# Kernel tuning notes

Measured on AMD Instinct MI355X. Metric: run time of the kernel, lower is better.

Reference implementation:

```python
import jax, jax.numpy as jnp
import numpy as np

B, Q, K, DQ, DK, DV, H = 4, 256, 1024, 512, 512, 512, 128
MASK_VALUE = -1e6  # matches torch sequence_mask fill of -1000000.0


def setup_inputs() -> dict:
    key = jax.random.key(0)
    ks = jax.random.split(key, 7)
    q = jax.random.normal(ks[0], (B, Q, DQ), dtype=jnp.float32)
    k = jax.random.normal(ks[1], (B, K, DK), dtype=jnp.float32)
    v = jax.random.normal(ks[2], (B, K, DV), dtype=jnp.float32)
    valid_lens = jax.random.randint(ks[3], (B,), 1, K + 1).astype(jnp.int64)
    # Linear weights stored torch-style as [out, in]
    w_q = jax.random.normal(ks[4], (H, DQ), dtype=jnp.float32) * 0.05
    w_k = jax.random.normal(ks[5], (H, DK), dtype=jnp.float32) * 0.05
    w_v = jax.random.normal(ks[6], (H,), dtype=jnp.float32) * 0.05
    return {"q": q, "k": k, "v": v, "valid_lens": valid_lens,
            "w_q": w_q, "w_k": w_k, "w_v": w_v}


def reference(q, k, v, valid_lens, w_q, w_k, w_v):
    qh = jnp.einsum("bqd,hd->bqh", q, w_q)              # [B,Q,H]
    kh = jnp.einsum("bkd,hd->bkh", k, w_k)              # [B,K,H]
    feats = jnp.tanh(qh[:, :, None, :] + kh[:, None, :, :])  # [B,Q,K,H]
    scores = jnp.einsum("bqkh,h->bqk", feats, w_v)      # [B,Q,K]
    mask = jnp.arange(K)[None, None, :] < valid_lens[:, None, None]
    scores = jnp.where(mask, scores, MASK_VALUE)
    attn = jax.nn.softmax(scores, axis=-1)              # dropout is identity (p=0)
    return jnp.einsum("bqk,bkv->bqv", attn, v)          # [B,Q,DV]
```

## Files before the change

### kernel.cpp

```cpp
#include <hip/hip_runtime.h>

#define B_ 4
#define Q_ 256
#define K_ 1024
#define D_ 512
#define H_ 128
#define DV_ 512
#define SCALE 2.885390081777927f
#define LOG2E 1.4426950408889634f
#define N2LOG2E (-2.0f * 1.4426950408889634f)

__device__ __forceinline__ float sigl(float x) {
    return __builtin_amdgcn_rcpf(__builtin_amdgcn_exp2f(x) + 1.0f);
}

__global__ __launch_bounds__(256) void transpose_w(
    const float* __restrict__ wq, const float* __restrict__ wk,
    float* __restrict__ wt_q, float* __restrict__ wt_k)
{
    __shared__ float Ts[64][133];
    const int t = threadIdx.x, bid = blockIdx.x;
    const int m = bid >> 3, d0 = (bid & 7) * 64;
    const float* W  = m ? wk : wq;
    float*       WT = m ? wt_k : wt_q;
#pragma unroll
    for (int i = 0; i < 8; ++i) {
        int idx = i * 256 + t;
        int h = idx >> 4, dq = idx & 15;
        float4 v = *(const float4*)&W[(size_t)h * D_ + d0 + dq*4];
        Ts[dq*4+0][h] = v.x; Ts[dq*4+1][h] = v.y;
        Ts[dq*4+2][h] = v.z; Ts[dq*4+3][h] = v.w;
    }
    __syncthreads();
#pragma unroll
    for (int i = 0; i < 8; ++i) {
        int idx = i * 256 + t;
        int d = idx >> 5, h4 = idx & 31;
        *(float4*)&WT[(size_t)(d0 + d) * H_ + h4*4] = *(const float4*)&Ts[d][h4*4];
    }
}

__global__ __launch_bounds__(256) void proj2_kernel(
    const float* __restrict__ qin, const float* __restrict__ kin,
    const float* __restrict__ wt_q, const float* __restrict__ wt_k,
    const int* __restrict__ valid_lens,
    float* __restrict__ qh_s, float4* __restrict__ kh4)
{
    __shared__ float Xs[16][512];

    const int t = threadIdx.x, bid = blockIdx.x;
    const bool isQ = bid < 64;
    const float* X; const float* WT; int R0; int b = 0;
    if (isQ) { X = qin; WT = wt_q; R0 = bid * 16; }
    else {
        int kb = bid - 64;
        b  = kb >> 6;
        R0 = (kb & 63) * 16;
        if (R0 >= valid_lens[b]) return;
        X = kin + (size_t)b * K_ * D_;
        WT = wt_k;
    }

#pragma unroll
    for (int i = 0; i < 8; ++i) {
        int idx = i * 256 + t;
        int row = idx >> 7, d4 = idx & 127;
        *(float4*)&Xs[row][d4*4] = *(const float4*)&X[(size_t)(R0 + row) * D_ + d4*4];
    }
    __syncthreads();

    const int h4 = t & 31, rg = t >> 5;
    const int r0 = rg * 2;
    float4 c0 = make_float4(0,0,0,0), c1 = c0;

    const float* WTh = WT + h4*4;
    float4 w0 = *(const float4*)&WTh[0*H_];
    float4 w1 = *(const float4*)&WTh[1*H_];
    float4 w2 = *(const float4*)&WTh[2*H_];
    float4 w3 = *(const float4*)&WTh[3*H_];

#pragma unroll 2
    for (int d0 = 0; d0 < D_; d0 += 4) {
        float4 u0 = w0, u1 = w1, u2 = w2, u3 = w3;
        int dn = (d0 + 4 < D_) ? d0 + 4 : d0;
        w0 = *(const float4*)&WTh[(size_t)(dn+0) * H_];
        w1 = *(const float4*)&WTh[(size_t)(dn+1) * H_];
        w2 = *(const float4*)&WTh[(size_t)(dn+2) * H_];
        w3 = *(const float4*)&WTh[(size_t)(dn+3) * H_];
        float4 x0 = *(const float4*)&Xs[r0][d0];
        float4 x1 = *(const float4*)&Xs[r0+1][d0];
        c0.x += x0.x*u0.x + x0.y*u1.x + x0.z*u2.x + x0.w*u3.x;
        c0.y += x0.x*u0.y + x0.y*u1.y + x0.z*u2.y + x0.w*u3.y;
        c0.z += x0.x*u0.z + x0.y*u1.z + x0.z*u2.z + x0.w*u3.z;
        c0.w += x0.x*u0.w + x0.y*u1.w + x0.z*u2.w + x0.w*u3.w;
        c1.x += x1.x*u0.x + x1.y*u1.x + x1.z*u2.x + x1.w*u3.x;
        c1.y += x1.x*u0.y + x1.y*u1.y + x1.z*u2.y + x1.w*u3.y;
        c1.z += x1.x*u0.z + x1.y*u1.z + x1.z*u2.z + x1.w*u3.z;
        c1.w += x1.x*u0.w + x1.y*u1.w + x1.z*u2.w + x1.w*u3.w;
    }
    c0.x *= SCALE; c0.y *= SCALE; c0.z *= SCALE; c0.w *= SCALE;
    c1.x *= SCALE; c1.y *= SCALE; c1.z *= SCALE; c1.w *= SCALE;

    if (isQ) {
        *(float4*)&qh_s[(size_t)(R0 + r0)     * H_ + h4*4] = c0;
        *(float4*)&qh_s[(size_t)(R0 + r0 + 1) * H_ + h4*4] = c1;
    } else {
        kh4[(size_t)(b*32 + h4) * K_ + R0 + r0]     = c0;
        kh4[(size_t)(b*32 + h4) * K_ + R0 + r0 + 1] = c1;
    }
}

__global__ __launch_bounds__(256) void attn_part(
    const float* __restrict__ qh_s, const float4* __restrict__ kh4,
    const float* __restrict__ wvg,  const int* __restrict__ valid_lens,
    const float* __restrict__ vin,
    float* __restrict__ s_part, float4* __restrict__ o_part)
{
    __shared__ float  qv[512];
    __shared__ float  wvs[128];
    __shared__ float  ptmp[4][128];
    __shared__ float  p[4][128];
    __shared__ float  sred[2][4];
    __shared__ float4 otmp[4][128];

    const int t   = threadIdx.x;
    const int bid = blockIdx.x;
    const int qt  = bid & 63, b = (bid >> 6) & 3, kc = bid >> 8;
    const int q0  = qt * 4;
    const int vl  = valid_lens[b];
    const int kbase = kc * 128;
    if (kbase >= vl) return;
    const int klen = min(128, vl - kbase);

    qv[t]       = qh_s[(size_t)(b*Q_ + q0) * H_ + t];
    qv[t + 256] = qh_s[(size_t)(b*Q_ + q0) * H_ + t + 256];
    if (t < 128) wvs[t] = wvg[t];
    __syncthreads();

    const int k   = t & 127;
    const int hh  = t >> 7;
    const bool active = k < klen;

    float acc[4] = {0.f, 0.f, 0.f, 0.f};
    if (active) {
        const float4* khp = kh4 + (size_t)b * 32 * K_ + (kbase + k)
                          + (size_t)(hh * 16) * K_;
        const int hq0 = hh * 16;
        float4 kxn = khp[0];
#pragma unroll 4
        for (int i = 0; i < 16; ++i) {
            float4 kx = kxn;
            int ni = (i < 15) ? i + 1 : 15;
            kxn = khp[(size_t)ni * K_];
            const int hq = hq0 + i;
            float w4[4], q4[4][4];
            *(float4*)&w4[0] = *(const float4*)&wvs[hq*4];
#pragma unroll
            for (int qi = 0; qi < 4; ++qi)
                *(float4*)&q4[qi][0] = *(const float4*)&qv[qi*128 + hq*4];
            float kxa[4];
            *(float4*)&kxa[0] = kx;
#pragma unroll
            for (int j = 0; j < 4; ++j)
#pragma unroll
                for (int qi = 0; qi < 4; ++qi)
                    acc[qi] += w4[j] * sigl(q4[qi][j] + kxa[j]);
        }
    }
    if (hh == 1) {
#pragma unroll
        for (int qi = 0; qi < 4; ++qi) ptmp[qi][k] = acc[qi];
    }
    __syncthreads();

    float wsum = 0.f;
#pragma unroll
    for (int i = 0; i < 32; ++i) {
        float4 w = *(const float4*)&wvs[i*4];
        wsum += w.x + w.y + w.z + w.w;
    }
    const float C = wsum * LOG2E;

    float psum[4] = {0.f, 0.f, 0.f, 0.f};
    if (hh == 0) {
#pragma unroll
        for (int qi = 0; qi < 4; ++qi) {
            float a = acc[qi] + ptmp[qi][k];
            float e = active ? __builtin_amdgcn_exp2f(fmaf(a, N2LOG2E, C)) : 0.f;
            p[qi][k] = e;
            psum[qi] = e;
        }
#pragma unroll
        for (int off = 32; off > 0; off >>= 1)
#pragma unroll
            for (int qi = 0; qi < 4; ++qi) psum[qi] += __shfl_xor(psum[qi], off);
        if ((t & 63) == 0) {
#pragma unroll
            for (int qi = 0; qi < 4; ++qi) sred[t >> 6][qi] = psum[qi];
        }
    }
    __syncthreads();
    if (t < 4)
        s_part[(size_t)(b*Q_ + q0 + t) * 8 + kc] = sred[0][t] + sred[1][t];

    const int col  = t & 127;
    const int half = t >> 7;
    const int kb2  = half * 64;
    const int ke2  = min(klen, kb2 + 64);
    const float4* vb = (const float4*)vin + (size_t)b * K_ * 128 + (size_t)kbase * 128;

    float4 o0 = make_float4(0,0,0,0), o1 = o0, o2 = o0, o3 = o0;
    int kk = kb2;
    const int nfull = (ke2 > kb2) ? ((ke2 - kb2) >> 2) : 0;
#define PVACC(oq, pq) \
    oq.x += pq.x*v0.x + pq.y*v1.x + pq.z*v2.x + pq.w*v3.x; \
    oq.y += pq.x*v0.y + pq.y*v1.y + pq.z*v2.y + pq.w*v3.y; \
    oq.z += pq.x*v0.z + pq.y*v1.z + pq.z*v2.z + pq.w*v3.z; \
    oq.w += pq.x*v0.w + pq.y*v1.w + pq.z*v2.w + pq.w*v3.w;
    if (nfull > 0) {
        float4 n0 = vb[(size_t)(kk+0)*128 + col];
        float4 n1 = vb[(size_t)(kk+1)*128 + col];
        float4 n2 = vb[(size_t)(kk+2)*128 + col];
        float4 n3 = vb[(size_t)(kk+3)*128 + col];
        for (int g = 0; g < nfull; ++g) {
            float4 v0 = n0, v1 = n1, v2 = n2, v3 = n3;
            int kn = kk + 4;
            if (g + 1 < nfull) {
                n0 = vb[(size_t)(kn+0)*128 + col];
                n1 = vb[(size_t)(kn+1)*128 + col];
                n2 = vb[(size_t)(kn+2)*128 + col];
                n3 = vb[(size_t)(kn+3)*128 + col];
            }
            float4 p0 = *(const float4*)&p[0][kk];
            float4 p1 = *(const float4*)&p[1][kk];
            float4 p2 = *(const float4*)&p[2][kk];
            float4 p3 = *(const float4*)&p[3][kk];
            PVACC(o0, p0) PVACC(o1, p1) PVACC(o2, p2) PVACC(o3, p3)
            kk = kn;
        }
    }
#undef PVACC
    for (; kk < ke2; ++kk) {
        float4 v0 = vb[(size_t)kk*128 + col];
        float pk;
        pk = p[0][kk]; o0.x += pk*v0.x; o0.y += pk*v0.y; o0.z += pk*v0.z; o0.w += pk*v0.w;
        pk = p[1][kk]; o1.x += pk*v0.x; o1.y += pk*v0.y; o1.z += pk*v0.z; o1.w += pk*v0.w;
        pk = p[2][kk]; o2.x += pk*v0.x; o2.y += pk*v0.y; o2.z += pk*v0.z; o2.w += pk*v0.w;
        pk = p[3][kk]; o3.x += pk*v0.x; o3.y += pk*v0.y; o3.z += pk*v0.z; o3.w += pk*v0.w;
    }

    if (half == 1) {
        otmp[0][col] = o0; otmp[1][col] = o1; otmp[2][col] = o2; otmp[3][col] = o3;
    }
    __syncthreads();
    if (half == 0) {
        float4 r;
        r = otmp[0][col]; o0.x += r.x; o0.y += r.y; o0.z += r.z; o0.w += r.w;
        r = otmp[1][col]; o1.x += r.x; o1.y += r.y; o1.z += r.z; o1.w += r.w;
        r = otmp[2][col]; o2.x += r.x; o2.y += r.y; o2.z += r.z; o2.w += r.w;
        r = otmp[3][col]; o3.x += r.x; o3.y += r.y; o3.z += r.z; o3.w += r.w;
        float4 os[4] = {o0, o1, o2, o3};
#pragma unroll
        for (int qi = 0; qi < 4; ++qi)
            o_part[((size_t)kc * 1024 + (b*Q_ + q0 + qi)) * 128 + col] = os[qi];
    }
}

__global__ __launch_bounds__(256) void finalize_kernel(
    const float4* __restrict__ o_part, const float* __restrict__ s_part,
    const int* __restrict__ valid_lens, float4* __restrict__ out)
{
    int gid = blockIdx.x * 256 + threadIdx.x;
    int row = gid >> 7, col = gid & 127;
    int b = row >> 8;
    int nch = (valid_lens[b] + 127) >> 7;
    float ssum = 0.f;
    float4 o = make_float4(0,0,0,0);
    for (int ch = 0; ch < nch; ++ch) {
        ssum += s_part[(size_t)row * 8 + ch];
        float4 r = o_part[((size_t)ch * 1024 + row) * 128 + col];
        o.x += r.x; o.y += r.y; o.z += r.z; o.w += r.w;
    }
    float rs = __builtin_amdgcn_rcpf(ssum);
    out[gid] = make_float4(o.x*rs, o.y*rs, o.z*rs, o.w*rs);
}

extern "C" void kernel_launch(void* const* d_in, const int* in_sizes, int n_in,
                              void* d_out, int out_size, void* d_ws, size_t ws_size,
                              hipStream_t stream)
{
    const float* q  = (const float*)d_in[0];
    const float* k  = (const float*)d_in[1];
    const float* v  = (const float*)d_in[2];
    const int*   vl = (const int*)d_in[3];
    const float* wq = (const float*)d_in[4];
    const float* wk = (const float*)d_in[5];
    const float* wv = (const float*)d_in[6];
    float* out = (float*)d_out;

    float* wt_q  = (float*)d_ws;
    float* wt_k  = wt_q  + D_*H_;
    float* qh_s  = wt_k  + D_*H_;
    float* kh4   = qh_s  + (size_t)B_*Q_*H_;
    float* s_prt = kh4   + (size_t)B_*H_*K_;
    float* o_prt = s_prt + (size_t)B_*Q_*8;

    transpose_w    <<<dim3(16),   dim3(256), 0, stream>>>(wq, wk, wt_q, wt_k);
    proj2_kernel   <<<dim3(320),  dim3(256), 0, stream>>>(q, k, wt_q, wt_k, vl, qh_s, (float4*)kh4);
    attn_part      <<<dim3(2048), dim3(256), 0, stream>>>(qh_s, (const float4*)kh4, wv, vl, v, s_prt, (float4*)o_prt);
    finalize_kernel<<<dim3(512),  dim3(256), 0, stream>>>((const float4*)o_prt, s_prt, vl, (float4*)out);
}
```

Before: 138.4 us.

## Split-K register-tiled projection GEMM and 8-query attention tiles

Replaces the weight transpose plus row-wise projection with a split-K 128x128 tiled GEMM: each block stages a 64-deep slice of X and W in shared memory, each thread computes an 8x8 register tile, and a separate reduce kernel sums the eight partial slices, applies the scale and writes the q/k layouts. The attention kernel now processes 8 queries per block instead of 4, halving the grid and doubling reuse of each loaded kh and V element. The cost is an extra partial-sum buffer round trip through global memory, more registers and shared memory per attention block, and fewer blocks to spread across the device.

```diff
diff --git a/kernel.cpp b/kernel.cpp
--- a/kernel.cpp
+++ b/kernel.cpp
@@ -14,100 +14,92 @@
     return __builtin_amdgcn_rcpf(__builtin_amdgcn_exp2f(x) + 1.0f);
 }
 
-__global__ __launch_bounds__(256) void transpose_w(
-    const float* __restrict__ wq, const float* __restrict__ wk,
-    float* __restrict__ wt_q, float* __restrict__ wt_k)
-{
-    __shared__ float Ts[64][133];
+__global__ __launch_bounds__(256) void proj_part(
+    const float* __restrict__ qin, const float* __restrict__ kin,
+    const float* __restrict__ wq,  const float* __restrict__ wk,
+    const int* __restrict__ valid_lens, float* __restrict__ psum)
+{
+    __shared__ float Xs[64][132];
+    __shared__ float Ws[64][132];
+
     const int t = threadIdx.x, bid = blockIdx.x;
-    const int m = bid >> 3, d0 = (bid & 7) * 64;
-    const float* W  = m ? wk : wq;
-    float*       WT = m ? wt_k : wt_q;
+    const int tile = bid % 40, ds = bid / 40;
+    const int d0 = ds * 64;
+    const float* X; const float* W;
+    if (tile < 8) { X = qin + (size_t)tile * 128 * D_; W = wq; }
+    else {
+        int kt = tile - 8, b = kt >> 3, kr = (kt & 7) * 128;
+        if (kr >= valid_lens[b]) return;
+        X = kin + ((size_t)b * K_ + kr) * D_;
+        W = wk;
+    }
+    const int R0 = tile * 128;
+
 #pragma unroll
     for (int i = 0; i < 8; ++i) {
-        int idx = i * 256 + t;
-        int h = idx >> 4, dq = idx & 15;
-        float4 v = *(const float4*)&W[(size_t)h * D_ + d0 + dq*4];
-        Ts[dq*4+0][h] = v.x; Ts[dq*4+1][h] = v.y;
-        Ts[dq*4+2][h] = v.z; Ts[dq*4+3][h] = v.w;
-    }
-    __syncthreads();
+        int idx = t + i * 256;
+        int row = idx >> 4, dq = (idx & 15) * 4;
+        float4 xv = *(const float4*)&X[(size_t)row * D_ + d0 + dq];
+        Xs[dq+0][row] = xv.x; Xs[dq+1][row] = xv.y;
+        Xs[dq+2][row] = xv.z; Xs[dq+3][row] = xv.w;
+    }
 #pragma unroll
     for (int i = 0; i < 8; ++i) {
-        int idx = i * 256 + t;
-        int d = idx >> 5, h4 = idx & 31;
-        *(float4*)&WT[(size_t)(d0 + d) * H_ + h4*4] = *(const float4*)&Ts[d][h4*4];
-    }
-}
-
-__global__ __launch_bounds__(256) void proj2_kernel(
-    const float* __restrict__ qin, const float* __restrict__ kin,
-    const float* __restrict__ wt_q, const float* __restrict__ wt_k,
-    const int* __restrict__ valid_lens,
+        int idx = t + i * 256;
+        int h = idx >> 4, dq = (idx & 15) * 4;
+        float4 wv = *(const float4*)&W[(size_t)h * D_ + d0 + dq];
+        Ws[dq+0][h] = wv.x; Ws[dq+1][h] = wv.y;
+        Ws[dq+2][h] = wv.z; Ws[dq+3][h] = wv.w;
+    }
+    __syncthreads();
+
+    const int wid = t >> 6, lane = t & 63;
+    const int r0 = (wid >> 1) * 64 + (lane >> 3) * 8;
+    const int h0 = (wid & 1)  * 64 + (lane & 7)  * 8;
+    float c[8][8] = {};
+
+#pragma unroll 8
+    for (int kk = 0; kk < 64; ++kk) {
+        float xr[8], wr[8];
+        *(float4*)&xr[0] = *(const float4*)&Xs[kk][r0];
+        *(float4*)&xr[4] = *(const float4*)&Xs[kk][r0 + 4];
+        *(float4*)&wr[0] = *(const float4*)&Ws[kk][h0];
+        *(float4*)&wr[4] = *(const float4*)&Ws[kk][h0 + 4];
+#pragma unroll
+        for (int i = 0; i < 8; ++i)
+#pragma unroll
+            for (int j = 0; j < 8; ++j) c[i][j] += xr[i] * wr[j];
+    }
+
+    float* outp = psum + ((size_t)ds * 5120 + R0) * 128;
+#pragma unroll
+    for (int i = 0; i < 8; ++i) {
+        *(float4*)&outp[(size_t)(r0 + i) * 128 + h0]     = *(const float4*)&c[i][0];
+        *(float4*)&outp[(size_t)(r0 + i) * 128 + h0 + 4] = *(const float4*)&c[i][4];
+    }
+}
+
+__global__ __launch_bounds__(256) void proj_reduce(
+    const float* __restrict__ psum, const int* __restrict__ valid_lens,
     float* __restrict__ qh_s, float4* __restrict__ kh4)
 {
-    __shared__ float Xs[16][512];
-
-    const int t = threadIdx.x, bid = blockIdx.x;
-    const bool isQ = bid < 64;
-    const float* X; const float* WT; int R0; int b = 0;
-    if (isQ) { X = qin; WT = wt_q; R0 = bid * 16; }
-    else {
-        int kb = bid - 64;
-        b  = kb >> 6;
-        R0 = (kb & 63) * 16;
-        if (R0 >= valid_lens[b]) return;
-        X = kin + (size_t)b * K_ * D_;
-        WT = wt_k;
-    }
-
-#pragma unroll
-    for (int i = 0; i < 8; ++i) {
-        int idx = i * 256 + t;
-        int row = idx >> 7, d4 = idx & 127;
-        *(float4*)&Xs[row][d4*4] = *(const float4*)&X[(size_t)(R0 + row) * D_ + d4*4];
-    }
-    __syncthreads();
-
-    const int h4 = t & 31, rg = t >> 5;
-    const int r0 = rg * 2;
-    float4 c0 = make_float4(0,0,0,0), c1 = c0;
-
-    const float* WTh = WT + h4*4;
-    float4 w0 = *(const float4*)&WTh[0*H_];
-    float4 w1 = *(const float4*)&WTh[1*H_];
-    float4 w2 = *(const float4*)&WTh[2*H_];
-    float4 w3 = *(const float4*)&WTh[3*H_];
-
-#pragma unroll 2
-    for (int d0 = 0; d0 < D_; d0 += 4) {
-        float4 u0 = w0, u1 = w1, u2 = w2, u3 = w3;
-        int dn = (d0 + 4 < D_) ? d0 + 4 : d0;
-        w0 = *(const float4*)&WTh[(size_t)(dn+0) * H_];
-        w1 = *(const float4*)&WTh[(size_t)(dn+1) * H_];
-        w2 = *(const float4*)&WTh[(size_t)(dn+2) * H_];
-        w3 = *(const float4*)&WTh[(size_t)(dn+3) * H_];
-        float4 x0 = *(const float4*)&Xs[r0][d0];
-        float4 x1 = *(const float4*)&Xs[r0+1][d0];
-        c0.x += x0.x*u0.x + x0.y*u1.x + x0.z*u2.x + x0.w*u3.x;
-        c0.y += x0.x*u0.y + x0.y*u1.y + x0.z*u2.y + x0.w*u3.y;
-        c0.z += x0.x*u0.z + x0.y*u1.z + x0.z*u2.z + x0.w*u3.z;
-        c0.w += x0.x*u0.w + x0.y*u1.w + x0.z*u2.w + x0.w*u3.w;
-        c1.x += x1.x*u0.x + x1.y*u1.x + x1.z*u2.x + x1.w*u3.x;
-        c1.y += x1.x*u0.y + x1.y*u1.y + x1.z*u2.y + x1.w*u3.y;
-        c1.z += x1.x*u0.z + x1.y*u1.z + x1.z*u2.z + x1.w*u3.z;
-        c1.w += x1.x*u0.w + x1.y*u1.w + x1.z*u2.w + x1.w*u3.w;
-    }
-    c0.x *= SCALE; c0.y *= SCALE; c0.z *= SCALE; c0.w *= SCALE;
-    c1.x *= SCALE; c1.y *= SCALE; c1.z *= SCALE; c1.w *= SCALE;
-
-    if (isQ) {
-        *(float4*)&qh_s[(size_t)(R0 + r0)     * H_ + h4*4] = c0;
-        *(float4*)&qh_s[(size_t)(R0 + r0 + 1) * H_ + h4*4] = c1;
-    } else {
-        kh4[(size_t)(b*32 + h4) * K_ + R0 + r0]     = c0;
-        kh4[(size_t)(b*32 + h4) * K_ + R0 + r0 + 1] = c1;
-    }
+    int gid = blockIdx.x * 256 + threadIdx.x;
+    int row = gid >> 5, c4 = gid & 31;
+    int b = 0, kk = 0;
+    if (row >= 1024) {
+        int r = row - 1024;
+        b = r >> 10; kk = r & 1023;
+        if (kk >= valid_lens[b]) return;
+    }
+    float4 s = make_float4(0.f, 0.f, 0.f, 0.f);
+#pragma unroll
+    for (int ds = 0; ds < 8; ++ds) {
+        float4 v = *(const float4*)&psum[((size_t)ds * 5120 + row) * 128 + c4 * 4];
+        s.x += v.x; s.y += v.y; s.z += v.z; s.w += v.w;
+    }
+    s.x *= SCALE; s.y *= SCALE; s.z *= SCALE; s.w *= SCALE;
+    if (row < 1024) *(float4*)&qh_s[(size_t)row * 128 + c4 * 4] = s;
+    else            kh4[((size_t)(b * 32 + c4)) * K_ + kk] = s;
 }
 
 __global__ __launch_bounds__(256) void attn_part(
@@ -116,32 +108,33 @@
     const float* __restrict__ vin,
     float* __restrict__ s_part, float4* __restrict__ o_part)
 {
-    __shared__ float  qv[512];
+    __shared__ float  qv[1024];
     __shared__ float  wvs[128];
-    __shared__ float  ptmp[4][128];
-    __shared__ float  p[4][128];
-    __shared__ float  sred[2][4];
-    __shared__ float4 otmp[4][128];
+    __shared__ float  ptmp[8][128];
+    __shared__ float  p[8][128];
+    __shared__ float  sred[2][8];
+    __shared__ float4 otmp[8][128];
 
     const int t   = threadIdx.x;
     const int bid = blockIdx.x;
-    const int qt  = bid & 63, b = (bid >> 6) & 3, kc = bid >> 8;
-    const int q0  = qt * 4;
+    const int qt  = bid & 31, b = (bid >> 5) & 3, kc = bid >> 7;
+    const int q0  = qt * 8;
     const int vl  = valid_lens[b];
     const int kbase = kc * 128;
     if (kbase >= vl) return;
     const int klen = min(128, vl - kbase);
 
-    qv[t]       = qh_s[(size_t)(b*Q_ + q0) * H_ + t];
-    qv[t + 256] = qh_s[(size_t)(b*Q_ + q0) * H_ + t + 256];
+#pragma unroll
+    for (int i = 0; i < 4; ++i)
+        qv[t + i * 256] = qh_s[(size_t)(b*Q_ + q0) * H_ + t + i * 256];
     if (t < 128) wvs[t] = wvg[t];
     __syncthreads();
 
-    const int k   = t & 127;
-    const int hh  = t >> 7;
+    const int k  = t & 127;
+    const int hh = t >> 7;
     const bool active = k < klen;
 
-    float acc[4] = {0.f, 0.f, 0.f, 0.f};
+    float acc[8] = {};
     if (active) {
         const float4* khp = kh4 + (size_t)b * 32 * K_ + (kbase + k)
                           + (size_t)(hh * 16) * K_;
@@ -153,23 +146,22 @@
             int ni = (i < 15) ? i + 1 : 15;
             kxn = khp[(size_t)ni * K_];
             const int hq = hq0 + i;
-            float w4[4], q4[4][4];
-            *(float4*)&w4[0] = *(const float4*)&wvs[hq*4];
-#pragma unroll
-            for (int qi = 0; qi < 4; ++qi)
-                *(float4*)&q4[qi][0] = *(const float4*)&qv[qi*128 + hq*4];
-            float kxa[4];
+            float w4[4], kxa[4];
+            *(float4*)&w4[0]  = *(const float4*)&wvs[hq*4];
             *(float4*)&kxa[0] = kx;
 #pragma unroll
-            for (int j = 0; j < 4; ++j)
-#pragma unroll
-                for (int qi = 0; qi < 4; ++qi)
-                    acc[qi] += w4[j] * sigl(q4[qi][j] + kxa[j]);
+            for (int qi = 0; qi < 8; ++qi) {
+                float q4[4];
+                *(float4*)&q4[0] = *(const float4*)&qv[qi*128 + hq*4];
+#pragma unroll
+                for (int j = 0; j < 4; ++j)
+                    acc[qi] += w4[j] * sigl(q4[j] + kxa[j]);
+            }
         }
     }
     if (hh == 1) {
 #pragma unroll
-        for (int qi = 0; qi < 4; ++qi) ptmp[qi][k] = acc[qi];
+        for (int qi = 0; qi < 8; ++qi) ptmp[qi][k] = acc[qi];
     }
     __syncthreads();
 
@@ -181,26 +173,26 @@
     }
     const float C = wsum * LOG2E;
 
-    float psum[4] = {0.f, 0.f, 0.f, 0.f};
     if (hh == 0) {
-#pragma unroll
-        for (int qi = 0; qi < 4; ++qi) {
+        float psum8[8];
+#pragma unroll
+        for (int qi = 0; qi < 8; ++qi) {
             float a = acc[qi] + ptmp[qi][k];
             float e = active ? __builtin_amdgcn_exp2f(fmaf(a, N2LOG2E, C)) : 0.f;
             p[qi][k] = e;
-            psum[qi] = e;
+            psum8[qi] = e;
         }
 #pragma unroll
         for (int off = 32; off > 0; off >>= 1)
 #pragma unroll
-            for (int qi = 0; qi < 4; ++qi) psum[qi] += __shfl_xor(psum[qi], off);
+            for (int qi = 0; qi < 8; ++qi) psum8[qi] += __shfl_xor(psum8[qi], off);
         if ((t & 63) == 0) {
 #pragma unroll
-            for (int qi = 0; qi < 4; ++qi) sred[t >> 6][qi] = psum[qi];
-        }
-    }
-    __syncthreads();
-    if (t < 4)
+            for (int qi = 0; qi < 8; ++qi) sred[t >> 6][qi] = psum8[qi];
+        }
+    }
+    __syncthreads();
+    if (t < 8)
         s_part[(size_t)(b*Q_ + q0 + t) * 8 + kc] = sred[0][t] + sred[1][t];
 
     const int col  = t & 127;
@@ -209,14 +201,12 @@
     const int ke2  = min(klen, kb2 + 64);
     const float4* vb = (const float4*)vin + (size_t)b * K_ * 128 + (size_t)kbase * 128;
 
-    float4 o0 = make_float4(0,0,0,0), o1 = o0, o2 = o0, o3 = o0;
+    float4 o[8];
+#pragma unroll
+    for (int qi = 0; qi < 8; ++qi) o[qi] = make_float4(0.f, 0.f, 0.f, 0.f);
+
     int kk = kb2;
     const int nfull = (ke2 > kb2) ? ((ke2 - kb2) >> 2) : 0;
-#define PVACC(oq, pq) \
-    oq.x += pq.x*v0.x + pq.y*v1.x + pq.z*v2.x + pq.w*v3.x; \
-    oq.y += pq.x*v0.y + pq.y*v1.y + pq.z*v2.y + pq.w*v3.y; \
-    oq.z += pq.x*v0.z + pq.y*v1.z + pq.z*v2.z + pq.w*v3.z; \
-    oq.w += pq.x*v0.w + pq.y*v1.w + pq.z*v2.w + pq.w*v3.w;
     if (nfull > 0) {
         float4 n0 = vb[(size_t)(kk+0)*128 + col];
         float4 n1 = vb[(size_t)(kk+1)*128 + col];
@@ -231,38 +221,39 @@
                 n2 = vb[(size_t)(kn+2)*128 + col];
                 n3 = vb[(size_t)(kn+3)*128 + col];
             }
-            float4 p0 = *(const float4*)&p[0][kk];
-            float4 p1 = *(const float4*)&p[1][kk];
-            float4 p2 = *(const float4*)&p[2][kk];
-            float4 p3 = *(const float4*)&p[3][kk];
-            PVACC(o0, p0) PVACC(o1, p1) PVACC(o2, p2) PVACC(o3, p3)
+#pragma unroll
+            for (int qi = 0; qi < 8; ++qi) {
+                float4 pq = *(const float4*)&p[qi][kk];
+                o[qi].x += pq.x*v0.x + pq.y*v1.x + pq.z*v2.x + pq.w*v3.x;
+                o[qi].y += pq.x*v0.y + pq.y*v1.y + pq.z*v2.y + pq.w*v3.y;
+                o[qi].z += pq.x*v0.z + pq.y*v1.z + pq.z*v2.z + pq.w*v3.z;
+                o[qi].w += pq.x*v0.w + pq.y*v1.w + pq.z*v2.w + pq.w*v3.w;
+            }
             kk = kn;
         }
     }
-#undef PVACC
     for (; kk < ke2; ++kk) {
         float4 v0 = vb[(size_t)kk*128 + col];
-        float pk;
-        pk = p[0][kk]; o0.x += pk*v0.x; o0.y += pk*v0.y; o0.z += pk*v0.z; o0.w += pk*v0.w;
-        pk = p[1][kk]; o1.x += pk*v0.x; o1.y += pk*v0.y; o1.z += pk*v0.z; o1.w += pk*v0.w;
-        pk = p[2][kk]; o2.x += pk*v0.x; o2.y += pk*v0.y; o2.z += pk*v0.z; o2.w += pk*v0.w;
-        pk = p[3][kk]; o3.x += pk*v0.x; o3.y += pk*v0.y; o3.z += pk*v0.z; o3.w += pk*v0.w;
+#pragma unroll
+        for (int qi = 0; qi < 8; ++qi) {
+            float pk = p[qi][kk];
+            o[qi].x += pk*v0.x; o[qi].y += pk*v0.y;
+            o[qi].z += pk*v0.z; o[qi].w += pk*v0.w;
+        }
     }
 
     if (half == 1) {
-        otmp[0][col] = o0; otmp[1][col] = o1; otmp[2][col] = o2; otmp[3][col] = o3;
+#pragma unroll
+        for (int qi = 0; qi < 8; ++qi) otmp[qi][col] = o[qi];
     }
     __syncthreads();
     if (half == 0) {
-        float4 r;
-        r = otmp[0][col]; o0.x += r.x; o0.y += r.y; o0.z += r.z; o0.w += r.w;
-        r = otmp[1][col]; o1.x += r.x; o1.y += r.y; o1.z += r.z; o1.w += r.w;
-        r = otmp[2][col]; o2.x += r.x; o2.y += r.y; o2.z += r.z; o2.w += r.w;
-        r = otmp[3][col]; o3.x += r.x; o3.y += r.y; o3.z += r.z; o3.w += r.w;
-        float4 os[4] = {o0, o1, o2, o3};
-#pragma unroll
-        for (int qi = 0; qi < 4; ++qi)
-            o_part[((size_t)kc * 1024 + (b*Q_ + q0 + qi)) * 128 + col] = os[qi];
+#pragma unroll
+        for (int qi = 0; qi < 8; ++qi) {
+            float4 r = otmp[qi][col];
+            o[qi].x += r.x; o[qi].y += r.y; o[qi].z += r.z; o[qi].w += r.w;
+            o_part[((size_t)kc * 1024 + (b*Q_ + q0 + qi)) * 128 + col] = o[qi];
+        }
     }
 }
 
@@ -275,7 +266,7 @@
     int b = row >> 8;
     int nch = (valid_lens[b] + 127) >> 7;
     float ssum = 0.f;
-    float4 o = make_float4(0,0,0,0);
+    float4 o = make_float4(0.f, 0.f, 0.f, 0.f);
     for (int ch = 0; ch < nch; ++ch) {
         ssum += s_part[(size_t)row * 8 + ch];
         float4 r = o_part[((size_t)ch * 1024 + row) * 128 + col];
@@ -298,15 +289,14 @@
     const float* wv = (const float*)d_in[6];
     float* out = (float*)d_out;
 
-    float* wt_q  = (float*)d_ws;
-    float* wt_k  = wt_q  + D_*H_;
-    float* qh_s  = wt_k  + D_*H_;
+    float* qh_s  = (float*)d_ws;
     float* kh4   = qh_s  + (size_t)B_*Q_*H_;
     float* s_prt = kh4   + (size_t)B_*H_*K_;
     float* o_prt = s_prt + (size_t)B_*Q_*8;
-
-    transpose_w    <<<dim3(16),   dim3(256), 0, stream>>>(wq, wk, wt_q, wt_k);
-    proj2_kernel   <<<dim3(320),  dim3(256), 0, stream>>>(q, k, wt_q, wt_k, vl, qh_s, (float4*)kh4);
-    attn_part      <<<dim3(2048), dim3(256), 0, stream>>>(qh_s, (const float4*)kh4, wv, vl, v, s_prt, (float4*)o_prt);
+    float* psum  = o_prt + (size_t)8*B_*Q_*DV_;
+
+    proj_part      <<<dim3(320),  dim3(256), 0, stream>>>(q, k, wq, wk, vl, psum);
+    proj_reduce    <<<dim3(640),  dim3(256), 0, stream>>>(psum, vl, qh_s, (float4*)kh4);
+    attn_part      <<<dim3(1024), dim3(256), 0, stream>>>(qh_s, (const float4*)kh4, wv, vl, v, s_prt, (float4*)o_prt);
     finalize_kernel<<<dim3(512),  dim3(256), 0, stream>>>((const float4*)o_prt, s_prt, vl, (float4*)out);
 }
```

Result: faster. 133.6 us (-3.5%).
